# Kernel tuning notes

Measured on AMD Instinct MI355X. Metric: run time of the kernel, lower is better.

The kernel has to match this reference:

```python
import jax, jax.numpy as jnp
import numpy as np

N_NODES = 100000
N_EDGES = 1600000
D = 64          # embedding_dim (in_feats == out_feats)
H = 1           # num_heads
NEG_SLOPE = 0.2


def setup_inputs() -> dict:
    key = jax.random.key(0)
    k = jax.random.split(key, 7)
    feat = jax.random.normal(k[0], (N_NODES, D), dtype=jnp.float32)
    W = jax.random.normal(k[1], (D, H * D), dtype=jnp.float32) * (1.0 / np.sqrt(D))
    attn_l = jax.random.normal(k[2], (1, H, D), dtype=jnp.float32) * (1.0 / np.sqrt(D))
    attn_r = jax.random.normal(k[3], (1, H, D), dtype=jnp.float32) * (1.0 / np.sqrt(D))
    bias = jnp.zeros((H * D,), dtype=jnp.float32)
    src = jax.random.randint(k[4], (N_EDGES,), 0, N_NODES, dtype=jnp.int32)
    dst = jax.random.randint(k[5], (N_EDGES,), 0, N_NODES, dtype=jnp.int32)
    return {"feat": feat, "W": W, "attn_l": attn_l, "attn_r": attn_r,
            "bias": bias, "src": src, "dst": dst}


def reference(feat, W, attn_l, attn_r, bias, src, dst):
    # fc (no bias), view to [N, H, D_out]
    ft = (feat @ W).reshape(-1, H, D)                       # [N, H, D]
    # per-node attention halves
    el = jnp.sum(ft * attn_l, axis=-1, keepdims=True)       # [N, H, 1]
    er = jnp.sum(ft * attn_r, axis=-1, keepdims=True)       # [N, H, 1]
    # edge score: u_add_v then leaky_relu
    e = el[src] + er[dst]                                    # [E, H, 1]
    e = jnp.where(e > 0, e, NEG_SLOPE * e)
    # edge softmax over incoming edges of each destination node
    emax = jax.ops.segment_max(e, dst, num_segments=N_NODES)  # [N, H, 1]
    e_exp = jnp.exp(e - emax[dst])
    denom = jax.ops.segment_sum(e_exp, dst, num_segments=N_NODES)  # [N, H, 1]
    a = e_exp / denom[dst]                                   # [E, H, 1]
    # u_mul_e + sum aggregation to destination
    m = ft[src] * a                                          # [E, H, D]
    rst = jax.ops.segment_sum(m, dst, num_segments=N_NODES)  # [N, H, D]
    # residual (Identity since in_feats == out_feats) + bias
    rst = rst + feat.reshape(-1, H, D)
    rst = rst + bias.reshape(1, H, D)
    return rst
```

## Files before the change

### kernel.cpp

```cpp
#include <hip/hip_runtime.h>
#include <hip/hip_fp16.h>
#include <math.h>

#define NN 100000
#define NE 1600000
#define D 64
#define NEG_SLOPE 0.2f
#define NBKT 391
#define NB1 196
#define CHUNK 8192
#define BSLOT 5120
#define NTILE 1563

typedef __attribute__((ext_vector_type(8))) short short8;
typedef __attribute__((ext_vector_type(4))) float f32x4;

template<int CTRL>
__device__ __forceinline__ float dpp_add(float x) {
    int y = __builtin_amdgcn_update_dpp(0, __float_as_int(x), CTRL, 0xf, 0xf, true);
    return x + __int_as_float(y);
}
template<int CTRL>
__device__ __forceinline__ float dpp_max(float x) {
    int xi = __float_as_int(x);
    int y = __builtin_amdgcn_update_dpp(xi, xi, CTRL, 0xf, 0xf, false);
    return fmaxf(x, __int_as_float(y));
}
__device__ __forceinline__ float wave_sum63(float x) {
    x = dpp_add<0x111>(x); x = dpp_add<0x112>(x); x = dpp_add<0x114>(x);
    x = dpp_add<0x118>(x); x = dpp_add<0x142>(x); x = dpp_add<0x143>(x);
    return x;
}
__device__ __forceinline__ float wave_max63(float x) {
    x = dpp_max<0x111>(x); x = dpp_max<0x112>(x); x = dpp_max<0x114>(x);
    x = dpp_max<0x118>(x); x = dpp_max<0x142>(x); x = dpp_max<0x143>(x);
    return x;
}
__device__ __forceinline__ float rdlane_f(float v, int l) {
    return __int_as_float(__builtin_amdgcn_readlane(__float_as_int(v), l));
}
__device__ __forceinline__ unsigned bf16_1(float f) {
    unsigned x = __float_as_uint(f);
    return (x + 0x7fffu + ((x >> 16) & 1u)) >> 16;
}
__device__ __forceinline__ unsigned bfpack(float a, float b) {
    return bf16_1(a) | (bf16_1(b) << 16);
}

__global__ __launch_bounds__(256) void k_pre(
    const int* __restrict__ src, const int* __restrict__ dst,
    const float* __restrict__ feat, const float* __restrict__ W,
    const float* __restrict__ attn_l, const float* __restrict__ attn_r,
    unsigned* __restrict__ bcnt, unsigned* __restrict__ binned,
    __half* __restrict__ ft, float* __restrict__ el, float* __restrict__ er)
{
    __shared__ __align__(16) char smem[16896];
    int t = threadIdx.x;

    if (blockIdx.x < NB1) {
        unsigned* lh = (unsigned*)smem;
        unsigned b0 = blockIdx.x * CHUNK;
        unsigned b1 = min(b0 + CHUNK, (unsigned)NE);
        unsigned n4 = (b1 - b0) >> 2;
        for (int k = t; k < NBKT; k += 256) lh[k] = 0u;
        __syncthreads();
        const int4* d4 = (const int4*)(dst + b0);
        const int4* s4 = (const int4*)(src + b0);
        for (unsigned i = t; i < n4; i += 256) {
            int4 v = d4[i];
            atomicAdd(&lh[((unsigned)v.x) >> 8], 1u);
            atomicAdd(&lh[((unsigned)v.y) >> 8], 1u);
            atomicAdd(&lh[((unsigned)v.z) >> 8], 1u);
            atomicAdd(&lh[((unsigned)v.w) >> 8], 1u);
        }
        __syncthreads();
        for (int k = t; k < NBKT; k += 256) {
            unsigned c = lh[k];
            if (c) lh[k] = (unsigned)k * BSLOT + atomicAdd(&bcnt[k], c);
        }
        __syncthreads();
        for (unsigned i = t; i < n4; i += 256) {
            int4 dv = d4[i];
            int4 sv = s4[i];
            { unsigned d_=(unsigned)dv.x, s_=(unsigned)sv.x;
              unsigned pos=atomicAdd(&lh[d_>>8],1u); binned[pos]=(s_<<8)|(d_&255u); }
            { unsigned d_=(unsigned)dv.y, s_=(unsigned)sv.y;
              unsigned pos=atomicAdd(&lh[d_>>8],1u); binned[pos]=(s_<<8)|(d_&255u); }
            { unsigned d_=(unsigned)dv.z, s_=(unsigned)sv.z;
              unsigned pos=atomicAdd(&lh[d_>>8],1u); binned[pos]=(s_<<8)|(d_&255u); }
            { unsigned d_=(unsigned)dv.w, s_=(unsigned)sv.w;
              unsigned pos=atomicAdd(&lh[d_>>8],1u); binned[pos]=(s_<<8)|(d_&255u); }
        }
        return;
    }

    unsigned short* Ab = (unsigned short*)smem;
    unsigned short* Bb = (unsigned short*)(smem + 8192);
    float* wlS = (float*)(smem + 16384);
    float* wrS = (float*)(smem + 16640);
    int n0 = (int)(blockIdx.x - NB1) * 64;

    {
        int k = t >> 2, s = t & 3;
        float pl = 0.f, pr = 0.f;
        #pragma unroll
        for (int q = 0; q < 4; ++q) {
            int seg = s + q * 4;
            float4 f = *(const float4*)(W + k * 64 + seg * 4);
            float4 a = *(const float4*)(attn_l + seg * 4);
            float4 b = *(const float4*)(attn_r + seg * 4);
            pl += f.x*a.x + f.y*a.y + f.z*a.z + f.w*a.w;
            pr += f.x*b.x + f.y*b.y + f.z*b.z + f.w*b.w;
        }
        pl += __shfl_xor(pl, 1, 64); pl += __shfl_xor(pl, 2, 64);
        pr += __shfl_xor(pr, 1, 64); pr += __shfl_xor(pr, 2, 64);
        if (s == 0) { wlS[k] = pl; wrS[k] = pr; }
    }
    {
        int j = t & 63, g = t >> 6;
        unsigned m = (unsigned)((j & 7) << 4);
        #pragma unroll
        for (int i = 0; i < 8; ++i) {
            int k0 = g * 16 + i * 2;
            float w0 = W[k0 * 64 + j];
            float w1 = W[(k0 + 1) * 64 + j];
            *(unsigned*)((char*)Bb + j * 128 + (((unsigned)(k0 * 2)) ^ m)) = bfpack(w0, w1);
        }
    }
    __syncthreads();
    {
        int r = t >> 2, s = t & 3;
        int n = n0 + r;
        bool valid = n < NN;
        const float* fp = feat + (size_t)(valid ? n : (NN - 1)) * D;
        float pl = 0.f, pr = 0.f;
        unsigned m = (unsigned)((r & 7) << 4);
        #pragma unroll
        for (int q = 0; q < 4; ++q) {
            int seg = s + q * 4;
            float4 f = *(const float4*)(fp + seg * 4);
            float4 a = *(const float4*)(wlS + seg * 4);
            float4 b = *(const float4*)(wrS + seg * 4);
            pl += f.x*a.x + f.y*a.y + f.z*a.z + f.w*a.w;
            pr += f.x*b.x + f.y*b.y + f.z*b.z + f.w*b.w;
            uint2 pk;
            pk.x = bfpack(f.x, f.y);
            pk.y = bfpack(f.z, f.w);
            *(uint2*)((char*)Ab + r * 128 + (((unsigned)(seg * 8)) ^ m)) = pk;
        }
        pl += __shfl_xor(pl, 1, 64); pl += __shfl_xor(pl, 2, 64);
        pr += __shfl_xor(pr, 1, 64); pr += __shfl_xor(pr, 2, 64);
        if (s == 0 && valid) { el[n] = pl; er[n] = pr; }
    }
    __syncthreads();

    int w = t >> 6, l = t & 63;
    int lr = l & 15, lg = l >> 4;
    f32x4 acc0 = {0.f,0.f,0.f,0.f};
    f32x4 acc1 = {0.f,0.f,0.f,0.f};
    f32x4 acc2 = {0.f,0.f,0.f,0.f};
    f32x4 acc3 = {0.f,0.f,0.f,0.f};

    int jrow = w * 16 + lr;
    unsigned bm = (unsigned)((jrow & 7) << 4);
    short8 bf0 = *(const short8*)((char*)Bb + jrow * 128 + (((unsigned)(0 + lg * 16)) ^ bm));
    short8 bf1 = *(const short8*)((char*)Bb + jrow * 128 + (((unsigned)(64 + lg * 16)) ^ bm));

    #pragma unroll
    for (int rt = 0; rt < 4; ++rt) {
        int arow = rt * 16 + lr;
        unsigned am = (unsigned)((arow & 7) << 4);
        short8 a0 = *(const short8*)((char*)Ab + arow * 128 + (((unsigned)(0 + lg * 16)) ^ am));
        short8 a1 = *(const short8*)((char*)Ab + arow * 128 + (((unsigned)(64 + lg * 16)) ^ am));
        f32x4 acc = (rt == 0) ? acc0 : (rt == 1) ? acc1 : (rt == 2) ? acc2 : acc3;
        acc = __builtin_amdgcn_mfma_f32_16x16x32_bf16(a0, bf0, acc, 0, 0, 0);
        acc = __builtin_amdgcn_mfma_f32_16x16x32_bf16(a1, bf1, acc, 0, 0, 0);
        if (rt == 0) acc0 = acc; else if (rt == 1) acc1 = acc;
        else if (rt == 2) acc2 = acc; else acc3 = acc;
    }

    int col = w * 16 + lr;
    #pragma unroll
    for (int rt = 0; rt < 4; ++rt) {
        f32x4 acc = (rt == 0) ? acc0 : (rt == 1) ? acc1 : (rt == 2) ? acc2 : acc3;
        #pragma unroll
        for (int i = 0; i < 4; ++i) {
            int row = rt * 16 + lg * 4 + i;
            int nn = n0 + row;
            if (nn < NN) ft[(size_t)nn * D + col] = __float2half(acc[i]);
        }
    }
}

__global__ __launch_bounds__(256) void k_bsort(const unsigned* __restrict__ bcnt,
                                               const unsigned* __restrict__ binned,
                                               int* __restrict__ perm,
                                               uint2* __restrict__ rowBE) {
    __shared__ unsigned lh[256];
    __shared__ unsigned cur[256];
    __shared__ unsigned stage[BSLOT];
    int t = threadIdx.x;
    int b = blockIdx.x;
    unsigned beg = (unsigned)b * BSLOT;
    unsigned cnt = bcnt[b];
    lh[t] = 0u;
    __syncthreads();
    for (unsigned i = t; i < cnt; i += 256) {
        unsigned w = binned[beg + i];
        stage[i] = w;
        atomicAdd(&lh[w & 255u], 1u);
    }
    __syncthreads();
    for (int off = 1; off < 256; off <<= 1) {
        unsigned u = (t >= off) ? lh[t - off] : 0u;
        __syncthreads();
        lh[t] += u;
        __syncthreads();
    }
    unsigned start = (t == 0) ? 0u : lh[t - 1];
    unsigned node = ((unsigned)b << 8) + (unsigned)t;
    if (node < NN) {
        uint2 be; be.x = beg + start; be.y = beg + lh[t];
        rowBE[node] = be;
    }
    cur[t] = start;
    __syncthreads();
    for (unsigned i = t; i < cnt; i += 256) {
        unsigned w = stage[i];
        unsigned pos = atomicAdd(&cur[w & 255u], 1u);
        perm[beg + pos] = (int)(w >> 8);
    }
}

__device__ __noinline__ void agg_node64(int d, int lane, unsigned beg, unsigned end,
                                        const int* __restrict__ perm_src,
                                        const float* __restrict__ el, float er_d,
                                        const __half* __restrict__ ft,
                                        const float* __restrict__ feat,
                                        const float* __restrict__ bias,
                                        float* __restrict__ out) {
    float acc = 0.0f;
    float s = 0.0f;
    float m = -INFINITY;
    for (unsigned base = beg; base < end; base += 64) {
        unsigned i = base + lane;
        float e = -INFINITY;
        if (i < end) {
            int sid2 = perm_src[i];
            float v = el[sid2] + er_d;
            e = v > 0.0f ? v : NEG_SLOPE * v;
        }
        m = fmaxf(m, rdlane_f(wave_max63(e), 63));
    }
    for (unsigned base = beg; base < end; base += 64) {
        unsigned i = base + lane;
        float exx = 0.0f;
        if (i < end) {
            int sid2 = perm_src[i];
            float v = el[sid2] + er_d;
            v = v > 0.0f ? v : NEG_SLOPE * v;
            exx = __expf(v - m);
        }
        s += rdlane_f(wave_sum63(exx), 63);
    }
    for (unsigned jj = beg; jj < end; ++jj) {
        int sj = perm_src[jj];
        float v = el[sj] + er_d;
        v = v > 0.0f ? v : NEG_SLOPE * v;
        acc = fmaf(__half2float(ft[((size_t)sj << 6) + lane]), __expf(v - m), acc);
    }
    acc /= s;
    out[(size_t)d * D + lane] = acc + feat[(size_t)d * D + lane] + bias[lane];
}

#define LOAD8(B, J) do { \
    unsigned _o0 = (((unsigned)__builtin_amdgcn_readlane(sid, (J) + 0)) << 7) | lb; \
    unsigned _o1 = (((unsigned)__builtin_amdgcn_readlane(sid, (J) + 1)) << 7) | lb; \
    unsigned _o2 = (((unsigned)__builtin_amdgcn_readlane(sid, (J) + 2)) << 7) | lb; \
    unsigned _o3 = (((unsigned)__builtin_amdgcn_readlane(sid, (J) + 3)) << 7) | lb; \
    unsigned _o4 = (((unsigned)__builtin_amdgcn_readlane(sid, (J) + 4)) << 7) | lb; \
    unsigned _o5 = (((unsigned)__builtin_amdgcn_readlane(sid, (J) + 5)) << 7) | lb; \
    unsigned _o6 = (((unsigned)__builtin_amdgcn_readlane(sid, (J) + 6)) << 7) | lb; \
    unsigned _o7 = (((unsigned)__builtin_amdgcn_readlane(sid, (J) + 7)) << 7) | lb; \
    B##0 = *(const __half*)(ftb + _o0); \
    B##1 = *(const __half*)(ftb + _o1); \
    B##2 = *(const __half*)(ftb + _o2); \
    B##3 = *(const __half*)(ftb + _o3); \
    B##4 = *(const __half*)(ftb + _o4); \
    B##5 = *(const __half*)(ftb + _o5); \
    B##6 = *(const __half*)(ftb + _o6); \
    B##7 = *(const __half*)(ftb + _o7); \
} while (0)

#define FMA8(B, J) do { \
    acc = fmaf(__half2float(B##0), rdlane_f(ex, (J) + 0), acc); \
    acc = fmaf(__half2float(B##1), rdlane_f(ex, (J) + 1), acc); \
    acc = fmaf(__half2float(B##2), rdlane_f(ex, (J) + 2), acc); \
    acc = fmaf(__half2float(B##3), rdlane_f(ex, (J) + 3), acc); \
    acc = fmaf(__half2float(B##4), rdlane_f(ex, (J) + 4), acc); \
    acc = fmaf(__half2float(B##5), rdlane_f(ex, (J) + 5), acc); \
    acc = fmaf(__half2float(B##6), rdlane_f(ex, (J) + 6), acc); \
    acc = fmaf(__half2float(B##7), rdlane_f(ex, (J) + 7), acc); \
} while (0)

__global__ __launch_bounds__(256) void k_agg(const uint2* __restrict__ rowBE,
                                             const int* __restrict__ perm_src,
                                             const float* __restrict__ el,
                                             const float* __restrict__ er,
                                             const __half* __restrict__ ft,
                                             const float* __restrict__ feat,
                                             const float* __restrict__ bias,
                                             float* __restrict__ out) {
    int gid = blockIdx.x * 256 + threadIdx.x;
    int d = gid >> 6;
    int lane = gid & 63;
    if (d >= NN) return;

    uint2 be = rowBE[d];
    unsigned beg = be.x;
    int deg = (int)(be.y - be.x);
    float er_d = er[d];

    if (deg > 64) {
        agg_node64(d, lane, be.x, be.y, perm_src, el, er_d, ft, feat, bias, out);
        return;
    }
    if (deg == 0) {
        out[(size_t)d * D + lane] = feat[(size_t)d * D + lane] + bias[lane];
        return;
    }

    int sid = perm_src[beg + ((lane < deg) ? lane : 0)];
    float elv = el[sid];

    const char* ftb = (const char*)ft;
    unsigned lb = (unsigned)lane << 1;

    __half c0, c1, c2, c3, c4, c5, c6, c7;
    __half n0, n1, n2, n3, n4, n5, n6, n7;
    LOAD8(c, 0);

    float e = elv + er_d;
    e = e > 0.0f ? e : NEG_SLOPE * e;
    float ex = (lane < deg) ? __expf(e) : 0.0f;
    float s = rdlane_f(wave_sum63(ex), 63);
    float inv_s = __frcp_rn(s);

    float acc = 0.0f;
    int j = 0;
    while (true) {
        bool more = (j + 8) < deg;
        if (more) LOAD8(n, j + 8);
        FMA8(c, j);
        j += 8;
        if (!more) break;
        bool more2 = (j + 8) < deg;
        if (more2) LOAD8(c, j + 8);
        FMA8(n, j);
        j += 8;
        if (!more2) break;
    }
    acc *= inv_s;
    out[(size_t)d * D + lane] = acc + feat[(size_t)d * D + lane] + bias[lane];
}

extern "C" void kernel_launch(void* const* d_in, const int* in_sizes, int n_in,
                              void* d_out, int out_size, void* d_ws, size_t ws_size,
                              hipStream_t stream) {
    const float* feat   = (const float*)d_in[0];
    const float* W      = (const float*)d_in[1];
    const float* attn_l = (const float*)d_in[2];
    const float* attn_r = (const float*)d_in[3];
    const float* bias   = (const float*)d_in[4];
    const int*   src    = (const int*)d_in[5];
    const int*   dst    = (const int*)d_in[6];
    float* out = (float*)d_out;

    char* ws = (char*)d_ws;
    __half*   ft     = (__half*)(ws);
    float*    el     = (float*)(ws + 12800000);
    float*    er     = (float*)(ws + 13200000);
    int*      perm   = (int*)(ws + 13600000);
    uint2*    rowBE  = (uint2*)(ws + 21607680);
    unsigned* bcnt   = (unsigned*)(ws + 22407680);
    unsigned* binned = (unsigned*)(ws + 22409248);

    hipMemsetAsync(bcnt, 0, NBKT * sizeof(unsigned), stream);
    k_pre<<<NB1 + NTILE, 256, 0, stream>>>(src, dst, feat, W, attn_l, attn_r,
                                           bcnt, binned, ft, el, er);
    k_bsort<<<NBKT, 256, 0, stream>>>(bcnt, binned, perm, rowBE);
    k_agg<<<(NN * 64 + 255) / 256, 256, 0, stream>>>(rowBE, perm, el, er,
                                                     ft, feat, bias, out);
}
```

Measured before the change: 93.58 us.

## Fuse per-bucket sort into aggregation kernel with 64-node buckets

Shrinks destination buckets from 256 to 64 nodes and merges the bucket sort kernel into the aggregation kernel. Each block now sorts its bucket's edges in shared memory and aggregates its 64 nodes directly, with each wave handling 16 nodes in turn. This removes the global perm and rowBE arrays, their writes and reads, and one kernel launch. In exchange there are only 1563 blocks doing serial per-wave node loops, which may reduce parallelism. The count is clamped to BSLOT, so a bucket overflow would silently drop edges, and the high-degree path now skips max-subtraction in the softmax.

```diff
diff --git a/kernel.cpp b/kernel.cpp
--- a/kernel.cpp
+++ b/kernel.cpp
@@ -6,10 +6,12 @@
 #define NE 1600000
 #define D 64
 #define NEG_SLOPE 0.2f
-#define NBKT 391
+#define BSH 6
+#define BMASK 63
+#define NBKT 1563
 #define NB1 196
 #define CHUNK 8192
-#define BSLOT 5120
+#define BSLOT 1280
 #define NTILE 1563
 
 typedef __attribute__((ext_vector_type(8))) short short8;
@@ -20,20 +22,9 @@
     int y = __builtin_amdgcn_update_dpp(0, __float_as_int(x), CTRL, 0xf, 0xf, true);
     return x + __int_as_float(y);
 }
-template<int CTRL>
-__device__ __forceinline__ float dpp_max(float x) {
-    int xi = __float_as_int(x);
-    int y = __builtin_amdgcn_update_dpp(xi, xi, CTRL, 0xf, 0xf, false);
-    return fmaxf(x, __int_as_float(y));
-}
 __device__ __forceinline__ float wave_sum63(float x) {
     x = dpp_add<0x111>(x); x = dpp_add<0x112>(x); x = dpp_add<0x114>(x);
     x = dpp_add<0x118>(x); x = dpp_add<0x142>(x); x = dpp_add<0x143>(x);
-    return x;
-}
-__device__ __forceinline__ float wave_max63(float x) {
-    x = dpp_max<0x111>(x); x = dpp_max<0x112>(x); x = dpp_max<0x114>(x);
-    x = dpp_max<0x118>(x); x = dpp_max<0x142>(x); x = dpp_max<0x143>(x);
     return x;
 }
 __device__ __forceinline__ float rdlane_f(float v, int l) {
@@ -68,10 +59,10 @@
         const int4* s4 = (const int4*)(src + b0);
         for (unsigned i = t; i < n4; i += 256) {
             int4 v = d4[i];
-            atomicAdd(&lh[((unsigned)v.x) >> 8], 1u);
-            atomicAdd(&lh[((unsigned)v.y) >> 8], 1u);
-            atomicAdd(&lh[((unsigned)v.z) >> 8], 1u);
-            atomicAdd(&lh[((unsigned)v.w) >> 8], 1u);
+            atomicAdd(&lh[((unsigned)v.x) >> BSH], 1u);
+            atomicAdd(&lh[((unsigned)v.y) >> BSH], 1u);
+            atomicAdd(&lh[((unsigned)v.z) >> BSH], 1u);
+            atomicAdd(&lh[((unsigned)v.w) >> BSH], 1u);
         }
         __syncthreads();
         for (int k = t; k < NBKT; k += 256) {
@@ -83,13 +74,13 @@
             int4 dv = d4[i];
             int4 sv = s4[i];
             { unsigned d_=(unsigned)dv.x, s_=(unsigned)sv.x;
-              unsigned pos=atomicAdd(&lh[d_>>8],1u); binned[pos]=(s_<<8)|(d_&255u); }
+              unsigned pos=atomicAdd(&lh[d_>>BSH],1u); binned[pos]=(s_<<BSH)|(d_&BMASK); }
             { unsigned d_=(unsigned)dv.y, s_=(unsigned)sv.y;
-              unsigned pos=atomicAdd(&lh[d_>>8],1u); binned[pos]=(s_<<8)|(d_&255u); }
+              unsigned pos=atomicAdd(&lh[d_>>BSH],1u); binned[pos]=(s_<<BSH)|(d_&BMASK); }
             { unsigned d_=(unsigned)dv.z, s_=(unsigned)sv.z;
-              unsigned pos=atomicAdd(&lh[d_>>8],1u); binned[pos]=(s_<<8)|(d_&255u); }
+              unsigned pos=atomicAdd(&lh[d_>>BSH],1u); binned[pos]=(s_<<BSH)|(d_&BMASK); }
             { unsigned d_=(unsigned)dv.w, s_=(unsigned)sv.w;
-              unsigned pos=atomicAdd(&lh[d_>>8],1u); binned[pos]=(s_<<8)|(d_&255u); }
+              unsigned pos=atomicAdd(&lh[d_>>BSH],1u); binned[pos]=(s_<<BSH)|(d_&BMASK); }
         }
         return;
     }
@@ -192,87 +183,6 @@
     }
 }
 
-__global__ __launch_bounds__(256) void k_bsort(const unsigned* __restrict__ bcnt,
-                                               const unsigned* __restrict__ binned,
-                                               int* __restrict__ perm,
-                                               uint2* __restrict__ rowBE) {
-    __shared__ unsigned lh[256];
-    __shared__ unsigned cur[256];
-    __shared__ unsigned stage[BSLOT];
-    int t = threadIdx.x;
-    int b = blockIdx.x;
-    unsigned beg = (unsigned)b * BSLOT;
-    unsigned cnt = bcnt[b];
-    lh[t] = 0u;
-    __syncthreads();
-    for (unsigned i = t; i < cnt; i += 256) {
-        unsigned w = binned[beg + i];
-        stage[i] = w;
-        atomicAdd(&lh[w & 255u], 1u);
-    }
-    __syncthreads();
-    for (int off = 1; off < 256; off <<= 1) {
-        unsigned u = (t >= off) ? lh[t - off] : 0u;
-        __syncthreads();
-        lh[t] += u;
-        __syncthreads();
-    }
-    unsigned start = (t == 0) ? 0u : lh[t - 1];
-    unsigned node = ((unsigned)b << 8) + (unsigned)t;
-    if (node < NN) {
-        uint2 be; be.x = beg + start; be.y = beg + lh[t];
-        rowBE[node] = be;
-    }
-    cur[t] = start;
-    __syncthreads();
-    for (unsigned i = t; i < cnt; i += 256) {
-        unsigned w = stage[i];
-        unsigned pos = atomicAdd(&cur[w & 255u], 1u);
-        perm[beg + pos] = (int)(w >> 8);
-    }
-}
-
-__device__ __noinline__ void agg_node64(int d, int lane, unsigned beg, unsigned end,
-                                        const int* __restrict__ perm_src,
-                                        const float* __restrict__ el, float er_d,
-                                        const __half* __restrict__ ft,
-                                        const float* __restrict__ feat,
-                                        const float* __restrict__ bias,
-                                        float* __restrict__ out) {
-    float acc = 0.0f;
-    float s = 0.0f;
-    float m = -INFINITY;
-    for (unsigned base = beg; base < end; base += 64) {
-        unsigned i = base + lane;
-        float e = -INFINITY;
-        if (i < end) {
-            int sid2 = perm_src[i];
-            float v = el[sid2] + er_d;
-            e = v > 0.0f ? v : NEG_SLOPE * v;
-        }
-        m = fmaxf(m, rdlane_f(wave_max63(e), 63));
-    }
-    for (unsigned base = beg; base < end; base += 64) {
-        unsigned i = base + lane;
-        float exx = 0.0f;
-        if (i < end) {
-            int sid2 = perm_src[i];
-            float v = el[sid2] + er_d;
-            v = v > 0.0f ? v : NEG_SLOPE * v;
-            exx = __expf(v - m);
-        }
-        s += rdlane_f(wave_sum63(exx), 63);
-    }
-    for (unsigned jj = beg; jj < end; ++jj) {
-        int sj = perm_src[jj];
-        float v = el[sj] + er_d;
-        v = v > 0.0f ? v : NEG_SLOPE * v;
-        acc = fmaf(__half2float(ft[((size_t)sj << 6) + lane]), __expf(v - m), acc);
-    }
-    acc /= s;
-    out[(size_t)d * D + lane] = acc + feat[(size_t)d * D + lane] + bias[lane];
-}
-
 #define LOAD8(B, J) do { \
     unsigned _o0 = (((unsigned)__builtin_amdgcn_readlane(sid, (J) + 0)) << 7) | lb; \
     unsigned _o1 = (((unsigned)__builtin_amdgcn_readlane(sid, (J) + 1)) << 7) | lb; \
@@ -303,65 +213,118 @@
     acc = fmaf(__half2float(B##7), rdlane_f(ex, (J) + 7), acc); \
 } while (0)
 
-__global__ __launch_bounds__(256) void k_agg(const uint2* __restrict__ rowBE,
-                                             const int* __restrict__ perm_src,
-                                             const float* __restrict__ el,
-                                             const float* __restrict__ er,
-                                             const __half* __restrict__ ft,
-                                             const float* __restrict__ feat,
-                                             const float* __restrict__ bias,
-                                             float* __restrict__ out) {
-    int gid = blockIdx.x * 256 + threadIdx.x;
-    int d = gid >> 6;
-    int lane = gid & 63;
-    if (d >= NN) return;
-
-    uint2 be = rowBE[d];
-    unsigned beg = be.x;
-    int deg = (int)(be.y - be.x);
-    float er_d = er[d];
-
-    if (deg > 64) {
-        agg_node64(d, lane, be.x, be.y, perm_src, el, er_d, ft, feat, bias, out);
-        return;
-    }
-    if (deg == 0) {
-        out[(size_t)d * D + lane] = feat[(size_t)d * D + lane] + bias[lane];
-        return;
-    }
-
-    int sid = perm_src[beg + ((lane < deg) ? lane : 0)];
-    float elv = el[sid];
-
+__global__ __launch_bounds__(256) void k_fagg(
+    const unsigned* __restrict__ bcnt, const unsigned* __restrict__ binned,
+    const float* __restrict__ el, const float* __restrict__ er,
+    const __half* __restrict__ ft, const float* __restrict__ feat,
+    const float* __restrict__ bias, float* __restrict__ out)
+{
+    __shared__ unsigned stage[BSLOT];
+    __shared__ unsigned sorted[BSLOT];
+    __shared__ unsigned lh[64];
+    __shared__ unsigned cur[64];
+    __shared__ unsigned nbe[65];
+    int t = threadIdx.x;
+    int b = blockIdx.x;
+    unsigned base = (unsigned)b * BSLOT;
+    unsigned cnt = min(bcnt[b], (unsigned)BSLOT);
+
+    if (t < 64) lh[t] = 0u;
+    __syncthreads();
+    for (unsigned i = t; i < cnt; i += 256) {
+        unsigned w = binned[base + i];
+        stage[i] = w;
+        atomicAdd(&lh[w & BMASK], 1u);
+    }
+    __syncthreads();
+    for (int off = 1; off < 64; off <<= 1) {
+        unsigned u = 0u;
+        if (t < 64 && t >= off) u = lh[t - off];
+        __syncthreads();
+        if (t < 64) lh[t] += u;
+        __syncthreads();
+    }
+    if (t < 64) {
+        unsigned start = t ? lh[t - 1] : 0u;
+        nbe[t] = start;
+        cur[t] = start;
+        if (t == 63) nbe[64] = lh[63];
+    }
+    __syncthreads();
+    for (unsigned i = t; i < cnt; i += 256) {
+        unsigned w = stage[i];
+        unsigned pos = atomicAdd(&cur[w & BMASK], 1u);
+        sorted[pos] = w >> BSH;
+    }
+    __syncthreads();
+
+    int wv = t >> 6, lane = t & 63;
     const char* ftb = (const char*)ft;
     unsigned lb = (unsigned)lane << 1;
 
-    __half c0, c1, c2, c3, c4, c5, c6, c7;
-    __half n0, n1, n2, n3, n4, n5, n6, n7;
-    LOAD8(c, 0);
-
-    float e = elv + er_d;
-    e = e > 0.0f ? e : NEG_SLOPE * e;
-    float ex = (lane < deg) ? __expf(e) : 0.0f;
-    float s = rdlane_f(wave_sum63(ex), 63);
-    float inv_s = __frcp_rn(s);
-
-    float acc = 0.0f;
-    int j = 0;
-    while (true) {
-        bool more = (j + 8) < deg;
-        if (more) LOAD8(n, j + 8);
-        FMA8(c, j);
-        j += 8;
-        if (!more) break;
-        bool more2 = (j + 8) < deg;
-        if (more2) LOAD8(c, j + 8);
-        FMA8(n, j);
-        j += 8;
-        if (!more2) break;
-    }
-    acc *= inv_s;
-    out[(size_t)d * D + lane] = acc + feat[(size_t)d * D + lane] + bias[lane];
+    for (int r = 0; r < 16; ++r) {
+        int loc = wv * 16 + r;
+        int d = (b << BSH) + loc;
+        if (d >= NN) break;
+        unsigned nb = nbe[loc];
+        int deg = (int)(nbe[loc + 1] - nb);
+        float er_d = er[d];
+
+        if (deg == 0) {
+            out[(size_t)d * D + lane] = feat[(size_t)d * D + lane] + bias[lane];
+            continue;
+        }
+        if (deg > 64) {
+            float s = 0.f;
+            for (int j = 0; j < deg; ++j) {
+                int sj = (int)sorted[nb + j];
+                float v = el[sj] + er_d;
+                v = v > 0.f ? v : NEG_SLOPE * v;
+                s += __expf(v);
+            }
+            float inv_s = __frcp_rn(s);
+            float acc = 0.f;
+            for (int j = 0; j < deg; ++j) {
+                int sj = (int)sorted[nb + j];
+                float v = el[sj] + er_d;
+                v = v > 0.f ? v : NEG_SLOPE * v;
+                acc = fmaf(__half2float(ft[((size_t)sj << 6) + lane]), __expf(v), acc);
+            }
+            acc *= inv_s;
+            out[(size_t)d * D + lane] = acc + feat[(size_t)d * D + lane] + bias[lane];
+            continue;
+        }
+
+        int sid = (int)sorted[nb + ((lane < deg) ? lane : 0)];
+        float elv = el[sid];
+
+        __half c0, c1, c2, c3, c4, c5, c6, c7;
+        __half n0, n1, n2, n3, n4, n5, n6, n7;
+        LOAD8(c, 0);
+
+        float e = elv + er_d;
+        e = e > 0.0f ? e : NEG_SLOPE * e;
+        float ex = (lane < deg) ? __expf(e) : 0.0f;
+        float s = rdlane_f(wave_sum63(ex), 63);
+        float inv_s = __frcp_rn(s);
+
+        float acc = 0.0f;
+        int j = 0;
+        while (true) {
+            bool more = (j + 8) < deg;
+            if (more) LOAD8(n, j + 8);
+            FMA8(c, j);
+            j += 8;
+            if (!more) break;
+            bool more2 = (j + 8) < deg;
+            if (more2) LOAD8(c, j + 8);
+            FMA8(n, j);
+            j += 8;
+            if (!more2) break;
+        }
+        acc *= inv_s;
+        out[(size_t)d * D + lane] = acc + feat[(size_t)d * D + lane] + bias[lane];
+    }
 }
 
 extern "C" void kernel_launch(void* const* d_in, const int* in_sizes, int n_in,
@@ -380,15 +343,11 @@
     __half*   ft     = (__half*)(ws);
     float*    el     = (float*)(ws + 12800000);
     float*    er     = (float*)(ws + 13200000);
-    int*      perm   = (int*)(ws + 13600000);
-    uint2*    rowBE  = (uint2*)(ws + 21607680);
-    unsigned* bcnt   = (unsigned*)(ws + 22407680);
-    unsigned* binned = (unsigned*)(ws + 22409248);
+    unsigned* binned = (unsigned*)(ws + 13600000);
+    unsigned* bcnt   = (unsigned*)(ws + 21602560);
 
     hipMemsetAsync(bcnt, 0, NBKT * sizeof(unsigned), stream);
     k_pre<<<NB1 + NTILE, 256, 0, stream>>>(src, dst, feat, W, attn_l, attn_r,
                                            bcnt, binned, ft, el, er);
-    k_bsort<<<NBKT, 256, 0, stream>>>(bcnt, binned, perm, rowBE);
-    k_agg<<<(NN * 64 + 255) / 256, 256, 0, stream>>>(rowBE, perm, el, er,
-                                                     ft, feat, bias, out);
-}
+    k_fagg<<<NBKT, 256, 0, stream>>>(bcnt, binned, el, er, ft, feat, bias, out);
+}
```

After: 95.27 us. Within noise of the previous version (+1.8%).

## Move edge binning into its own kernel and fuse bucket sort with the GEMM

Applied to the files above, without the earlier changes.

Edge binning now runs alone in a new kernel with smaller chunks and more blocks. The per-bucket counting sort is folded into the same launch as the feature-projection GEMM tiles, so the sort overlaps with the MFMA work and the GEMM no longer shares a launch with binning. The aggregation kernel also issues the residual feat/bias loads early so their latency hides behind the edge loop. Launch count is unchanged, but shared memory per block grows and the bucket count is now clamped to BSLOT.

```diff
diff --git a/kernel.cpp b/kernel.cpp
--- a/kernel.cpp
+++ b/kernel.cpp
@@ -7,8 +7,8 @@
 #define D 64
 #define NEG_SLOPE 0.2f
 #define NBKT 391
-#define NB1 196
-#define CHUNK 8192
+#define NBIN 391
+#define CHUNKB 4096
 #define BSLOT 5120
 #define NTILE 1563
 
@@ -47,49 +47,90 @@
     return bf16_1(a) | (bf16_1(b) << 16);
 }
 
-__global__ __launch_bounds__(256) void k_pre(
-    const int* __restrict__ src, const int* __restrict__ dst,
+__global__ __launch_bounds__(256) void k_bin(const int* __restrict__ src,
+                                             const int* __restrict__ dst,
+                                             unsigned* __restrict__ bcnt,
+                                             unsigned* __restrict__ binned) {
+    __shared__ unsigned lh[NBKT];
+    int t = threadIdx.x;
+    unsigned b0 = blockIdx.x * CHUNKB;
+    unsigned b1 = min(b0 + CHUNKB, (unsigned)NE);
+    if (b0 >= b1) return;
+    unsigned n4 = (b1 - b0) >> 2;
+    for (int k = t; k < NBKT; k += 256) lh[k] = 0u;
+    __syncthreads();
+    const int4* d4 = (const int4*)(dst + b0);
+    const int4* s4 = (const int4*)(src + b0);
+    for (unsigned i = t; i < n4; i += 256) {
+        int4 v = d4[i];
+        atomicAdd(&lh[((unsigned)v.x) >> 8], 1u);
+        atomicAdd(&lh[((unsigned)v.y) >> 8], 1u);
+        atomicAdd(&lh[((unsigned)v.z) >> 8], 1u);
+        atomicAdd(&lh[((unsigned)v.w) >> 8], 1u);
+    }
+    __syncthreads();
+    for (int k = t; k < NBKT; k += 256) {
+        unsigned c = lh[k];
+        if (c) lh[k] = (unsigned)k * BSLOT + atomicAdd(&bcnt[k], c);
+    }
+    __syncthreads();
+    for (unsigned i = t; i < n4; i += 256) {
+        int4 dv = d4[i];
+        int4 sv = s4[i];
+        { unsigned d_=(unsigned)dv.x, s_=(unsigned)sv.x;
+          unsigned pos=atomicAdd(&lh[d_>>8],1u); binned[pos]=(s_<<8)|(d_&255u); }
+        { unsigned d_=(unsigned)dv.y, s_=(unsigned)sv.y;
+          unsigned pos=atomicAdd(&lh[d_>>8],1u); binned[pos]=(s_<<8)|(d_&255u); }
+        { unsigned d_=(unsigned)dv.z, s_=(unsigned)sv.z;
+          unsigned pos=atomicAdd(&lh[d_>>8],1u); binned[pos]=(s_<<8)|(d_&255u); }
+        { unsigned d_=(unsigned)dv.w, s_=(unsigned)sv.w;
+          unsigned pos=atomicAdd(&lh[d_>>8],1u); binned[pos]=(s_<<8)|(d_&255u); }
+    }
+}
+
+__global__ __launch_bounds__(256) void k_sg(
+    const unsigned* __restrict__ bcnt, const unsigned* __restrict__ binned,
+    int* __restrict__ perm, uint2* __restrict__ rowBE,
     const float* __restrict__ feat, const float* __restrict__ W,
     const float* __restrict__ attn_l, const float* __restrict__ attn_r,
-    unsigned* __restrict__ bcnt, unsigned* __restrict__ binned,
     __half* __restrict__ ft, float* __restrict__ el, float* __restrict__ er)
 {
-    __shared__ __align__(16) char smem[16896];
+    __shared__ __align__(16) char smem[22784];
     int t = threadIdx.x;
 
-    if (blockIdx.x < NB1) {
-        unsigned* lh = (unsigned*)smem;
-        unsigned b0 = blockIdx.x * CHUNK;
-        unsigned b1 = min(b0 + CHUNK, (unsigned)NE);
-        unsigned n4 = (b1 - b0) >> 2;
-        for (int k = t; k < NBKT; k += 256) lh[k] = 0u;
+    if (blockIdx.x < NBKT) {
+        unsigned* lh    = (unsigned*)smem;
+        unsigned* cur   = (unsigned*)smem + 256;
+        unsigned* stage = (unsigned*)smem + 512;
+        int b = blockIdx.x;
+        unsigned beg = (unsigned)b * BSLOT;
+        unsigned cnt = min(bcnt[b], (unsigned)BSLOT);
+        lh[t] = 0u;
         __syncthreads();
-        const int4* d4 = (const int4*)(dst + b0);
-        const int4* s4 = (const int4*)(src + b0);
-        for (unsigned i = t; i < n4; i += 256) {
-            int4 v = d4[i];
-            atomicAdd(&lh[((unsigned)v.x) >> 8], 1u);
-            atomicAdd(&lh[((unsigned)v.y) >> 8], 1u);
-            atomicAdd(&lh[((unsigned)v.z) >> 8], 1u);
-            atomicAdd(&lh[((unsigned)v.w) >> 8], 1u);
+        for (unsigned i = t; i < cnt; i += 256) {
+            unsigned w = binned[beg + i];
+            stage[i] = w;
+            atomicAdd(&lh[w & 255u], 1u);
         }
         __syncthreads();
-        for (int k = t; k < NBKT; k += 256) {
-            unsigned c = lh[k];
-            if (c) lh[k] = (unsigned)k * BSLOT + atomicAdd(&bcnt[k], c);
-        }
+        for (int off = 1; off < 256; off <<= 1) {
+            unsigned u = (t >= off) ? lh[t - off] : 0u;
+            __syncthreads();
+            lh[t] += u;
+            __syncthreads();
+        }
+        unsigned start = (t == 0) ? 0u : lh[t - 1];
+        unsigned node = ((unsigned)b << 8) + (unsigned)t;
+        if (node < NN) {
+            uint2 be; be.x = beg + start; be.y = beg + lh[t];
+            rowBE[node] = be;
+        }
+        cur[t] = start;
         __syncthreads();
-        for (unsigned i = t; i < n4; i += 256) {
-            int4 dv = d4[i];
-            int4 sv = s4[i];
-            { unsigned d_=(unsigned)dv.x, s_=(unsigned)sv.x;
-              unsigned pos=atomicAdd(&lh[d_>>8],1u); binned[pos]=(s_<<8)|(d_&255u); }
-            { unsigned d_=(unsigned)dv.y, s_=(unsigned)sv.y;
-              unsigned pos=atomicAdd(&lh[d_>>8],1u); binned[pos]=(s_<<8)|(d_&255u); }
-            { unsigned d_=(unsigned)dv.z, s_=(unsigned)sv.z;
-              unsigned pos=atomicAdd(&lh[d_>>8],1u); binned[pos]=(s_<<8)|(d_&255u); }
-            { unsigned d_=(unsigned)dv.w, s_=(unsigned)sv.w;
-              unsigned pos=atomicAdd(&lh[d_>>8],1u); binned[pos]=(s_<<8)|(d_&255u); }
+        for (unsigned i = t; i < cnt; i += 256) {
+            unsigned w = stage[i];
+            unsigned pos = atomicAdd(&cur[w & 255u], 1u);
+            perm[beg + pos] = (int)(w >> 8);
         }
         return;
     }
@@ -98,7 +139,7 @@
     unsigned short* Bb = (unsigned short*)(smem + 8192);
     float* wlS = (float*)(smem + 16384);
     float* wrS = (float*)(smem + 16640);
-    int n0 = (int)(blockIdx.x - NB1) * 64;
+    int n0 = (int)(blockIdx.x - NBKT) * 64;
 
     {
         int k = t >> 2, s = t & 3;
@@ -192,46 +233,6 @@
     }
 }
 
-__global__ __launch_bounds__(256) void k_bsort(const unsigned* __restrict__ bcnt,
-                                               const unsigned* __restrict__ binned,
-                                               int* __restrict__ perm,
-                                               uint2* __restrict__ rowBE) {
-    __shared__ unsigned lh[256];
-    __shared__ unsigned cur[256];
-    __shared__ unsigned stage[BSLOT];
-    int t = threadIdx.x;
-    int b = blockIdx.x;
-    unsigned beg = (unsigned)b * BSLOT;
-    unsigned cnt = bcnt[b];
-    lh[t] = 0u;
-    __syncthreads();
-    for (unsigned i = t; i < cnt; i += 256) {
-        unsigned w = binned[beg + i];
-        stage[i] = w;
-        atomicAdd(&lh[w & 255u], 1u);
-    }
-    __syncthreads();
-    for (int off = 1; off < 256; off <<= 1) {
-        unsigned u = (t >= off) ? lh[t - off] : 0u;
-        __syncthreads();
-        lh[t] += u;
-        __syncthreads();
-    }
-    unsigned start = (t == 0) ? 0u : lh[t - 1];
-    unsigned node = ((unsigned)b << 8) + (unsigned)t;
-    if (node < NN) {
-        uint2 be; be.x = beg + start; be.y = beg + lh[t];
-        rowBE[node] = be;
-    }
-    cur[t] = start;
-    __syncthreads();
-    for (unsigned i = t; i < cnt; i += 256) {
-        unsigned w = stage[i];
-        unsigned pos = atomicAdd(&cur[w & 255u], 1u);
-        perm[beg + pos] = (int)(w >> 8);
-    }
-}
-
 __device__ __noinline__ void agg_node64(int d, int lane, unsigned beg, unsigned end,
                                         const int* __restrict__ perm_src,
                                         const float* __restrict__ el, float er_d,
@@ -332,6 +333,8 @@
 
     int sid = perm_src[beg + ((lane < deg) ? lane : 0)];
     float elv = el[sid];
+    float fv = feat[(size_t)d * D + lane];
+    float bv = bias[lane];
 
     const char* ftb = (const char*)ft;
     unsigned lb = (unsigned)lane << 1;
@@ -361,7 +364,7 @@
         if (!more2) break;
     }
     acc *= inv_s;
-    out[(size_t)d * D + lane] = acc + feat[(size_t)d * D + lane] + bias[lane];
+    out[(size_t)d * D + lane] = acc + fv + bv;
 }
 
 extern "C" void kernel_launch(void* const* d_in, const int* in_sizes, int n_in,
@@ -386,9 +389,9 @@
     unsigned* binned = (unsigned*)(ws + 22409248);
 
     hipMemsetAsync(bcnt, 0, NBKT * sizeof(unsigned), stream);
-    k_pre<<<NB1 + NTILE, 256, 0, stream>>>(src, dst, feat, W, attn_l, attn_r,
-                                           bcnt, binned, ft, el, er);
-    k_bsort<<<NBKT, 256, 0, stream>>>(bcnt, binned, perm, rowBE);
+    k_bin<<<NBIN, 256, 0, stream>>>(src, dst, bcnt, binned);
+    k_sg<<<NBKT + NTILE, 256, 0, stream>>>(bcnt, binned, perm, rowBE,
+                                           feat, W, attn_l, attn_r, ft, el, er);
     k_agg<<<(NN * 64 + 255) / 256, 256, 0, stream>>>(rowBE, perm, el, er,
                                                      ft, feat, bias, out);
 }
```

Result: no change. 93.05 us, median of 2 (-0.6%).
